# Performance work log

Measured on AMD Instinct MI355X. Metric: run time of the kernel, lower is better.

## Reference

```python
import jax, jax.numpy as jnp
import numpy as np

L = 16          # num_slices
RMIN, RMAX = 0.4, 0.9
B_, C_, H_, W_, N_ = 2, 4, 64, 64, 64   # n = 64 scan steps, last dim of x = N_*L


def setup_inputs() -> dict:
    key = jax.random.key(0)
    k = jax.random.split(key, 8)
    u1 = jax.random.uniform(k[0], (L,), dtype=jnp.float32)
    u2 = jax.random.uniform(k[1], (L,), dtype=jnp.float32)
    theta = 2.0 * np.pi * u2
    nu_log = jnp.log(-0.5 * jnp.log(u1 * (RMAX ** 2 - RMIN ** 2) + RMIN ** 2))
    # torch.complex(exp(-exp(nu_log)), theta): real part = modulus-like term, imag = theta
    Lambda_re = jnp.exp(-jnp.exp(nu_log))
    Lambda_im = theta
    B_re = jax.random.normal(k[2], (L, L), dtype=jnp.float32)
    B_im = jax.random.normal(k[3], (L, L), dtype=jnp.float32)
    C_re = jax.random.normal(k[4], (L, L), dtype=jnp.float32)
    C_im = jax.random.normal(k[5], (L, L), dtype=jnp.float32)
    D = jax.random.normal(k[6], (L, L), dtype=jnp.float32)
    x = jax.random.normal(k[7], (B_, C_, H_, W_, N_ * L), dtype=jnp.float32)
    return {"x": x, "Lambda_re": Lambda_re, "Lambda_im": Lambda_im,
            "B_re": B_re, "B_im": B_im, "C_re": C_re, "C_im": C_im, "D": D}


def reference(x, Lambda_re, Lambda_im, B_re, B_im, C_re, C_im, D):
    l = Lambda_re.shape[0]
    b, c, h, w, nl = x.shape
    n = nl // l
    img = x.reshape(b, c, h, w, n, l)                       # 'b c h w (n l) -> b c h w n l'
    Lam = jax.lax.complex(Lambda_re, Lambda_im)             # (l,) complex64
    Bc = jax.lax.complex(B_re, B_im)                        # (l,l) complex64
    Cc = jax.lax.complex(C_re, C_im)
    out = img.astype(jnp.complex64)
    # Faithful Hillis-Steele loop with op(x, y) = Lambda*x + B @ y
    for d in range(1, int(np.log2(n)) + 1):
        step = 2 ** (d - 1)
        left = out[..., : n - step, :]
        right = out[..., step:, :]
        new = left * Lam + jnp.einsum('kl,bchwnl->bchwnk', Bc, right)
        out = jnp.concatenate([out[..., :step, :], new], axis=-2)
    y = jnp.real(jnp.einsum('kl,bchwnl->bchwnk', Cc, out)) \
        + jnp.einsum('kl,bchwnl->bchwnk', D, img)
    return y
```

## Files before the change

### kernel.cpp

```cpp
#include <hip/hip_runtime.h>


namespace {

typedef __attribute__((ext_vector_type(8))) short short8v;
typedef __attribute__((ext_vector_type(4))) float f32x4;

__device__ inline unsigned short f2bf_rne(float f) {
    unsigned u = __builtin_bit_cast(unsigned, f);
    u += 0x7fffu + ((u >> 16) & 1u);
    return (unsigned short)(u >> 16);
}

__device__ inline void gld_lds16(const unsigned short* g, unsigned short* l) {
    __builtin_amdgcn_global_load_lds(
        (const __attribute__((address_space(1))) unsigned int*)g,
        (__attribute__((address_space(3))) unsigned int*)l, 16, 0, 0);
}


__global__ __launch_bounds__(256) void build_w_kernel(
    const float* __restrict__ Lre, const float* __restrict__ Lim,
    const float* __restrict__ Bre, const float* __restrict__ Bim,
    const float* __restrict__ Cre, const float* __restrict__ Cim,
    const float* __restrict__ Dm,
    unsigned short* __restrict__ Wh)
{
    const int i = blockIdx.x >> 6, j = blockIdx.x & 63;
    const int t = threadIdx.x, k = t >> 4, l = t & 15;

    const int n_g = i * 16 + k;
    const int k_g = j * 16 + l;
    const size_t widx = (((size_t)((n_g >> 7) * 32 + (k_g >> 5))) << 12)
                      + (((k_g >> 3) & 3) << 10) + ((n_g & 127) << 3) + (k_g & 7);

    if (j > i) { Wh[widx] = 0; return; }

    __shared__ float2 Bs[16][16];
    __shared__ float2 M[16][16];
    Bs[k][l] = make_float2(Bre[t], Bim[t]);
    M[k][l]  = make_float2(k == l ? 1.f : 0.f, 0.f);
    const int delta = i - j;
    __syncthreads();

    #pragma unroll
    for (int d = 0; d < 6; ++d) {
        const int s = 1 << d;
        if (delta & s) {
            const float lr = Lre[k], li = Lim[k];
            const float2 m0 = M[k][l];
            M[k][l] = make_float2(lr * m0.x - li * m0.y, lr * m0.y + li * m0.x);
            __syncthreads();
        } else if (j + (delta & (s - 1)) >= s) {
            float2 acc = make_float2(0.f, 0.f);
            #pragma unroll
            for (int m = 0; m < 16; ++m) {
                const float2 b = Bs[k][m], v = M[m][l];
                acc.x += b.x * v.x - b.y * v.y;
                acc.y += b.x * v.y + b.y * v.x;
            }
            __syncthreads();
            M[k][l] = acc;
            __syncthreads();
        }
    }

    float w = 0.f;
    #pragma unroll
    for (int m = 0; m < 16; ++m) {
        const float2 v = M[m][l];
        w += Cre[k * 16 + m] * v.x - Cim[k * 16 + m] * v.y;
    }
    if (i == j) w += Dm[t];
    Wh[widx] = f2bf_rne(w);
}

__global__ __launch_bounds__(256) void gemm_fused_kernel(
    const float* __restrict__ X,
    const unsigned short* __restrict__ Wh,
    float* __restrict__ Y, int mtiles)
{
    __shared__ alignas(16) unsigned short sA[2][4096];
    __shared__ alignas(16) unsigned short sW[2][4096];

    const int bid = blockIdx.x;
    const int nb = 7 - bid / mtiles;
    const int mt = bid % mtiles;
    const int t = threadIdx.x;
    const int wid = t >> 6, lane = t & 63;
    const int wr = wid >> 1, wc = wid & 1;
    const int l15 = lane & 15, lg = lane >> 4;
    const int nk = (nb + 1) * 4;

    f32x4 acc[4][4] = {};

    const int arow = t & 127;
    const int ag0 = t >> 7;
    const float* xrow = X + (size_t)(mt * 128 + arow) * 1024;
    const int aoff0 = (ag0 << 10) + (arow << 3);
    const int aoff1 = ((ag0 + 2) << 10) + (arow << 3);

    float4 xr[4];
    auto x_issue = [&](int kc) {
        const float* s0 = xrow + kc * 32 + ag0 * 8;
        const float* s1 = s0 + 16;
        xr[0] = *reinterpret_cast<const float4*>(s0);
        xr[1] = *reinterpret_cast<const float4*>(s0 + 4);
        xr[2] = *reinterpret_cast<const float4*>(s1);
        xr[3] = *reinterpret_cast<const float4*>(s1 + 4);
    };
    auto cvt8 = [&](const float4& a, const float4& b) -> short8v {
        short8v r;
        r[0] = (short)f2bf_rne(a.x); r[1] = (short)f2bf_rne(a.y);
        r[2] = (short)f2bf_rne(a.z); r[3] = (short)f2bf_rne(a.w);
        r[4] = (short)f2bf_rne(b.x); r[5] = (short)f2bf_rne(b.y);
        r[6] = (short)f2bf_rne(b.z); r[7] = (short)f2bf_rne(b.w);
        return r;
    };
    auto x_write = [&](unsigned short* buf) {
        *reinterpret_cast<short8v*>(buf + aoff0) = cvt8(xr[0], xr[1]);
        *reinterpret_cast<short8v*>(buf + aoff1) = cvt8(xr[2], xr[3]);
    };
    auto w_issue = [&](unsigned short* buf, int kc) {
        const size_t wb = ((size_t)(nb * 32 + kc)) << 12;
        gld_lds16(Wh + wb + t * 8,        buf + t * 8);
        gld_lds16(Wh + wb + 2048 + t * 8, buf + 2048 + t * 8);
    };

    x_issue(0);
    w_issue(sW[0], 0);
    x_write(sA[0]);
    __syncthreads();

    int cur = 0;
    for (int kc = 0; kc < nk; ++kc) {
        const bool more = (kc + 1 < nk);
        if (more) {
            x_issue(kc + 1);
            w_issue(sW[cur ^ 1], kc + 1);
        }

        short8v ah[4], bh[4];
        #pragma unroll
        for (int mm = 0; mm < 4; ++mm) {
            const int o = (lg << 10) + ((wr * 64 + mm * 16 + l15) << 3);
            ah[mm] = *reinterpret_cast<const short8v*>(sA[cur] + o);
        }
        #pragma unroll
        for (int nn = 0; nn < 4; ++nn) {
            const int o = (lg << 10) + ((wc * 64 + nn * 16 + l15) << 3);
            bh[nn] = *reinterpret_cast<const short8v*>(sW[cur] + o);
        }
        #pragma unroll
        for (int mm = 0; mm < 4; ++mm) {
            #pragma unroll
            for (int nn = 0; nn < 4; ++nn) {
                acc[mm][nn] = __builtin_amdgcn_mfma_f32_16x16x32_bf16(
                    ah[mm], bh[nn], acc[mm][nn], 0, 0, 0);
            }
        }

        if (more) x_write(sA[cur ^ 1]);
        __syncthreads();
        cur ^= 1;
    }

    #pragma unroll
    for (int mm = 0; mm < 4; ++mm) {
        const int grow = mt * 128 + wr * 64 + mm * 16 + lg * 4;
        #pragma unroll
        for (int nn = 0; nn < 4; ++nn) {
            const int gcol = nb * 128 + wc * 64 + nn * 16 + l15;
            #pragma unroll
            for (int q = 0; q < 4; ++q)
                Y[(size_t)(grow + q) * 1024 + gcol] = acc[mm][nn][q];
        }
    }
}

}

extern "C" void kernel_launch(void* const* d_in, const int* in_sizes, int n_in,
                              void* d_out, int out_size, void* d_ws, size_t ws_size,
                              hipStream_t stream) {
    const float* x   = (const float*)d_in[0];
    const float* Lre = (const float*)d_in[1];
    const float* Lim = (const float*)d_in[2];
    const float* Bre = (const float*)d_in[3];
    const float* Bim = (const float*)d_in[4];
    const float* Cre = (const float*)d_in[5];
    const float* Cim = (const float*)d_in[6];
    const float* Dm  = (const float*)d_in[7];
    float* y = (float*)d_out;

    const int positions = in_sizes[0] / 1024;
    const int mtiles = positions / 128;

    unsigned short* Wh = (unsigned short*)d_ws;

    build_w_kernel<<<64 * 64, 256, 0, stream>>>(Lre, Lim, Bre, Bim, Cre, Cim, Dm, Wh);
    gemm_fused_kernel<<<mtiles * 8, 256, 0, stream>>>(x, Wh, y, mtiles);
}
```

Measured before the change: 119.8 us.

## Keep full bf16 X slab in LDS and sweep all output column blocks

Each block now loads a 64-row slab of X once, converts it to bf16 into padded LDS, and loops over all eight triangular output column blocks. This removes the repeated reads and conversion of X that the previous 2D grid did for every column block. The W fragments are streamed straight from global memory into registers with a 4-deep software prefetch instead of being staged in LDS. The trade-offs are 512-thread blocks with about 136KB of LDS each, which limits occupancy to one block per CU, and the triangular loop serialises uneven work inside each block.

```diff
diff --git a/kernel.cpp b/kernel.cpp
--- a/kernel.cpp
+++ b/kernel.cpp
@@ -10,12 +10,6 @@
     unsigned u = __builtin_bit_cast(unsigned, f);
     u += 0x7fffu + ((u >> 16) & 1u);
     return (unsigned short)(u >> 16);
-}
-
-__device__ inline void gld_lds16(const unsigned short* g, unsigned short* l) {
-    __builtin_amdgcn_global_load_lds(
-        (const __attribute__((address_space(1))) unsigned int*)g,
-        (__attribute__((address_space(3))) unsigned int*)l, 16, 0, 0);
 }
 
 
@@ -75,105 +69,97 @@
     Wh[widx] = f2bf_rne(w);
 }
 
-__global__ __launch_bounds__(256) void gemm_fused_kernel(
+__global__ __launch_bounds__(512) void gemm_persist_kernel(
     const float* __restrict__ X,
     const unsigned short* __restrict__ Wh,
-    float* __restrict__ Y, int mtiles)
+    float* __restrict__ Y)
 {
-    __shared__ alignas(16) unsigned short sA[2][4096];
-    __shared__ alignas(16) unsigned short sW[2][4096];
+    __shared__ alignas(16) unsigned short sA[128 * 544];
 
-    const int bid = blockIdx.x;
-    const int nb = 7 - bid / mtiles;
-    const int mt = bid % mtiles;
+    const int blk = blockIdx.x;
     const int t = threadIdx.x;
-    const int wid = t >> 6, lane = t & 63;
-    const int wr = wid >> 1, wc = wid & 1;
+    const int lane = t & 63;
+    const int w = t >> 6;
+    const int wr = w >> 2;
+    const int wcn = w & 3;
     const int l15 = lane & 15, lg = lane >> 4;
-    const int nk = (nb + 1) * 4;
 
-    f32x4 acc[4][4] = {};
-
-    const int arow = t & 127;
-    const int ag0 = t >> 7;
-    const float* xrow = X + (size_t)(mt * 128 + arow) * 1024;
-    const int aoff0 = (ag0 << 10) + (arow << 3);
-    const int aoff1 = ((ag0 + 2) << 10) + (arow << 3);
-
-    float4 xr[4];
-    auto x_issue = [&](int kc) {
-        const float* s0 = xrow + kc * 32 + ag0 * 8;
-        const float* s1 = s0 + 16;
-        xr[0] = *reinterpret_cast<const float4*>(s0);
-        xr[1] = *reinterpret_cast<const float4*>(s0 + 4);
-        xr[2] = *reinterpret_cast<const float4*>(s1);
-        xr[3] = *reinterpret_cast<const float4*>(s1 + 4);
-    };
-    auto cvt8 = [&](const float4& a, const float4& b) -> short8v {
-        short8v r;
-        r[0] = (short)f2bf_rne(a.x); r[1] = (short)f2bf_rne(a.y);
-        r[2] = (short)f2bf_rne(a.z); r[3] = (short)f2bf_rne(a.w);
-        r[4] = (short)f2bf_rne(b.x); r[5] = (short)f2bf_rne(b.y);
-        r[6] = (short)f2bf_rne(b.z); r[7] = (short)f2bf_rne(b.w);
-        return r;
-    };
-    auto x_write = [&](unsigned short* buf) {
-        *reinterpret_cast<short8v*>(buf + aoff0) = cvt8(xr[0], xr[1]);
-        *reinterpret_cast<short8v*>(buf + aoff1) = cvt8(xr[2], xr[3]);
-    };
-    auto w_issue = [&](unsigned short* buf, int kc) {
-        const size_t wb = ((size_t)(nb * 32 + kc)) << 12;
-        gld_lds16(Wh + wb + t * 8,        buf + t * 8);
-        gld_lds16(Wh + wb + 2048 + t * 8, buf + 2048 + t * 8);
-    };
-
-    x_issue(0);
-    w_issue(sW[0], 0);
-    x_write(sA[0]);
+    {
+        const float* xb = X + (size_t)blk * 65536;
+        #pragma unroll 4
+        for (int p = 0; p < 16; ++p) {
+            const int s = (p << 9) + t;
+            const int row = s >> 7, kg = s & 127;
+            const float* src = xb + (row << 10) + (kg << 3);
+            const float4 a = *reinterpret_cast<const float4*>(src);
+            const float4 b = *reinterpret_cast<const float4*>(src + 4);
+            short8v hv;
+            hv[0] = (short)f2bf_rne(a.x); hv[1] = (short)f2bf_rne(a.y);
+            hv[2] = (short)f2bf_rne(a.z); hv[3] = (short)f2bf_rne(a.w);
+            hv[4] = (short)f2bf_rne(b.x); hv[5] = (short)f2bf_rne(b.y);
+            hv[6] = (short)f2bf_rne(b.z); hv[7] = (short)f2bf_rne(b.w);
+            *reinterpret_cast<short8v*>(sA + kg * 544 + (row << 3)) = hv;
+        }
+    }
     __syncthreads();
 
-    int cur = 0;
-    for (int kc = 0; kc < nk; ++kc) {
-        const bool more = (kc + 1 < nk);
-        if (more) {
-            x_issue(kc + 1);
-            w_issue(sW[cur ^ 1], kc + 1);
+    int aof[2];
+    #pragma unroll
+    for (int mm = 0; mm < 2; ++mm) {
+        const int row = wr * 32 + mm * 16 + l15;
+        aof[mm] = lg * 544 + (row << 3);
+    }
+    int wfo[2];
+    #pragma unroll
+    for (int nn = 0; nn < 2; ++nn)
+        wfo[nn] = (lg << 10) + ((wcn * 32 + nn * 16 + l15) << 3);
+
+    for (int nb = 0; nb < 8; ++nb) {
+        const int nk = (nb + 1) * 4;
+        f32x4 acc[2][2] = {};
+
+        short8v b0[2], b1[2], b2[2], b3[2];
+        const unsigned short* wt = Wh + (((size_t)nb * 32) << 12);
+        auto LW = [&](short8v* bb, int kc) {
+            const unsigned short* p = wt + ((size_t)kc << 12);
+            bb[0] = *reinterpret_cast<const short8v*>(p + wfo[0]);
+            bb[1] = *reinterpret_cast<const short8v*>(p + wfo[1]);
+        };
+        auto MF = [&](const short8v* bb, int kc) {
+            short8v ah[2];
+            #pragma unroll
+            for (int mm = 0; mm < 2; ++mm)
+                ah[mm] = *reinterpret_cast<const short8v*>(sA + aof[mm] + kc * 2176);
+            #pragma unroll
+            for (int mm = 0; mm < 2; ++mm)
+                #pragma unroll
+                for (int nn = 0; nn < 2; ++nn)
+                    acc[mm][nn] = __builtin_amdgcn_mfma_f32_16x16x32_bf16(
+                        ah[mm], bb[nn], acc[mm][nn], 0, 0, 0);
+        };
+
+        LW(b0, 0); LW(b1, 1); LW(b2, 2); LW(b3, 3);
+        for (int kc = 0; kc < nk; kc += 4) {
+            MF(b0, kc);
+            if (kc + 4 < nk) LW(b0, kc + 4);
+            MF(b1, kc + 1);
+            if (kc + 5 < nk) LW(b1, kc + 5);
+            MF(b2, kc + 2);
+            if (kc + 6 < nk) LW(b2, kc + 6);
+            MF(b3, kc + 3);
+            if (kc + 7 < nk) LW(b3, kc + 7);
         }
 
-        short8v ah[4], bh[4];
         #pragma unroll
-        for (int mm = 0; mm < 4; ++mm) {
-            const int o = (lg << 10) + ((wr * 64 + mm * 16 + l15) << 3);
-            ah[mm] = *reinterpret_cast<const short8v*>(sA[cur] + o);
-        }
-        #pragma unroll
-        for (int nn = 0; nn < 4; ++nn) {
-            const int o = (lg << 10) + ((wc * 64 + nn * 16 + l15) << 3);
-            bh[nn] = *reinterpret_cast<const short8v*>(sW[cur] + o);
-        }
-        #pragma unroll
-        for (int mm = 0; mm < 4; ++mm) {
+        for (int mm = 0; mm < 2; ++mm) {
+            const int grow = blk * 64 + wr * 32 + mm * 16 + lg * 4;
             #pragma unroll
-            for (int nn = 0; nn < 4; ++nn) {
-                acc[mm][nn] = __builtin_amdgcn_mfma_f32_16x16x32_bf16(
-                    ah[mm], bh[nn], acc[mm][nn], 0, 0, 0);
+            for (int nn = 0; nn < 2; ++nn) {
+                const int gcol = nb * 128 + wcn * 32 + nn * 16 + l15;
+                #pragma unroll
+                for (int q = 0; q < 4; ++q)
+                    Y[(size_t)(grow + q) * 1024 + gcol] = acc[mm][nn][q];
             }
-        }
-
-        if (more) x_write(sA[cur ^ 1]);
-        __syncthreads();
-        cur ^= 1;
-    }
-
-    #pragma unroll
-    for (int mm = 0; mm < 4; ++mm) {
-        const int grow = mt * 128 + wr * 64 + mm * 16 + lg * 4;
-        #pragma unroll
-        for (int nn = 0; nn < 4; ++nn) {
-            const int gcol = nb * 128 + wc * 64 + nn * 16 + l15;
-            #pragma unroll
-            for (int q = 0; q < 4; ++q)
-                Y[(size_t)(grow + q) * 1024 + gcol] = acc[mm][nn][q];
         }
     }
 }
@@ -194,10 +180,10 @@
     float* y = (float*)d_out;
 
     const int positions = in_sizes[0] / 1024;
-    const int mtiles = positions / 128;
+    const int slabs = positions / 64;
 
     unsigned short* Wh = (unsigned short*)d_ws;
 
     build_w_kernel<<<64 * 64, 256, 0, stream>>>(Lre, Lim, Bre, Bim, Cre, Cim, Dm, Wh);
-    gemm_fused_kernel<<<mtiles * 8, 256, 0, stream>>>(x, Wh, y, mtiles);
+    gemm_persist_kernel<<<slabs, 512, 0, stream>>>(x, Wh, y);
 }
```

New measurement: 122.6 us. 1.02x slower.
